# Performance work log

Measured on AMD Instinct MI355X. Metric: run time of the kernel, lower is better.

The kernel has to match this reference:

```python
import jax, jax.numpy as jnp
import numpy as np

B, T, H = 2, 512, 256


def setup_inputs() -> dict:
    key = jax.random.key(0)
    k1, k2, k3, k4, k5 = jax.random.split(key, 5)
    scale = 1.0 / np.sqrt(H)
    Q = jax.random.normal(k1, (B, T, H), dtype=jnp.float32)
    K = jax.random.normal(k2, (B, T, H), dtype=jnp.float32)
    # torch nn.Linear weights: y = x @ W.T, W shape [out, in]
    Wq = jax.random.normal(k3, (H, H), dtype=jnp.float32) * scale
    Wk = jax.random.normal(k4, (H, H), dtype=jnp.float32) * scale
    v = jax.random.normal(k5, (H,), dtype=jnp.float32) * scale  # Linear(H,1) weight
    return {"Q": Q, "K": K, "Wq": Wq, "Wk": Wk, "v": v}


def reference(Q, K, Wq, Wk, v):
    # Project queries and keys: [B,T,H]
    Qp = jnp.einsum("bth,oh->bto", Q, Wq)
    Kp = jnp.einsum("bsh,oh->bso", K, Wk)
    # Additive (Bahdanau) scores: tanh over broadcast sum -> [B,T,T,H], then v-proj -> [B,T,T]
    e = jnp.tanh(Qp[:, :, None, :] + Kp[:, None, :, :])
    scores = jnp.einsum("btsh,h->bts", e, v)
    # Causal mask: query t may only attend to keys s <= t
    mask = jnp.tril(jnp.ones((T, T), dtype=bool))
    scores = jnp.where(mask[None, :, :], scores, jnp.float32(-1e9))
    alpha = jax.nn.softmax(scores, axis=-1)
    # Weighted sum of (raw) K values: [B,T,H]
    ctx = jnp.einsum("bts,bsh->bth", alpha, K)
    return ctx, alpha
```

## Files before the change

### kernel.cpp

```cpp
#include <hip/hip_runtime.h>

#define BB 2
#define TT 512
#define HH 256
#define NBT (BB * TT)

#define C2LOG2E 2.8853900817779268f

__global__ __launch_bounds__(256) void proj_kernel(
    const float* __restrict__ Q, const float* __restrict__ K,
    const float* __restrict__ Wq, const float* __restrict__ Wk,
    float* __restrict__ Eq, float* __restrict__ EkT)
{
    const int ROWS = 8;
    int grp = blockIdx.x;
    const int nQ = NBT / ROWS;
    bool isK = (grp >= nQ);
    int bt0 = (isK ? grp - nQ : grp) * ROWS;
    const float* X = isK ? K : Q;
    const float* W = isK ? Wk : Wq;

    int o = threadIdx.x;
    const float4* w4p = reinterpret_cast<const float4*>(W + o * HH);
    const float4* x4p = reinterpret_cast<const float4*>(X + bt0 * HH);

    float acc[ROWS] = {0.f, 0.f, 0.f, 0.f, 0.f, 0.f, 0.f, 0.f};
#pragma unroll 2
    for (int h4 = 0; h4 < HH / 4; ++h4) {
        float4 w4 = w4p[h4];
#pragma unroll
        for (int r = 0; r < ROWS; ++r) {
            float4 x4 = x4p[r * (HH / 4) + h4];
            acc[r] += x4.x * w4.x + x4.y * w4.y + x4.z * w4.z + x4.w * w4.w;
        }
    }
    if (!isK) {
#pragma unroll
        for (int r = 0; r < ROWS; ++r)
            Eq[(bt0 + r) * HH + o] = __builtin_amdgcn_exp2f(acc[r] * C2LOG2E);
    } else {
        int h4 = o >> 2, c = o & 3;
#pragma unroll
        for (int r = 0; r < ROWS; ++r)
            EkT[(h4 * NBT + bt0 + r) * 4 + c] = __builtin_amdgcn_exp2f(acc[r] * C2LOG2E);
    }
}

__global__ __launch_bounds__(512, 8) void attn_kernel(
    const float* __restrict__ Eq, const float* __restrict__ EkT,
    const float* __restrict__ Kraw, const float* __restrict__ v,
    float* __restrict__ ctx, float* __restrict__ alpha)
{
    int bt = blockIdx.x;
    int b = bt / TT;
    int idx = bt % TT;
    int t = (idx < 256) ? idx : 767 - idx;
    int btr = b * TT + t;
    int tid = threadIdx.x;

    __shared__ float eq_sh[HH];
    __shared__ float v2_sh[HH];
    __shared__ float al_sh[TT];
    __shared__ float red[8];
    __shared__ float4 cred[8][64];

    if (tid < HH) {
        eq_sh[tid] = Eq[btr * HH + tid];
        v2_sh[tid] = -2.0f * v[tid];
    }
    __syncthreads();

    const float4* q4p = reinterpret_cast<const float4*>(eq_sh);
    const float4* v4p = reinterpret_cast<const float4*>(v2_sh);

    float sc = -3.0e38f;
    if (tid <= t) {
        const float4* ek = reinterpret_cast<const float4*>(EkT) + (b * TT + tid);
        float a = 0.f;
#pragma unroll 4
        for (int h4 = 0; h4 < HH / 4; ++h4) {
            float4 e4 = ek[h4 * NBT];
            float4 q4 = q4p[h4];
            float4 vv = v4p[h4];
            float r0 = __builtin_amdgcn_rcpf(__builtin_fmaf(q4.x, e4.x, 1.0f));
            float r1 = __builtin_amdgcn_rcpf(__builtin_fmaf(q4.y, e4.y, 1.0f));
            float r2 = __builtin_amdgcn_rcpf(__builtin_fmaf(q4.z, e4.z, 1.0f));
            float r3 = __builtin_amdgcn_rcpf(__builtin_fmaf(q4.w, e4.w, 1.0f));
            a = __builtin_fmaf(vv.x, r0, a);
            a = __builtin_fmaf(vv.y, r1, a);
            a = __builtin_fmaf(vv.z, r2, a);
            a = __builtin_fmaf(vv.w, r3, a);
        }
        sc = a;
    }

    float m = sc;
#pragma unroll
    for (int off = 32; off > 0; off >>= 1)
        m = fmaxf(m, __shfl_xor(m, off));
    int wid = tid >> 6;
    if ((tid & 63) == 0) red[wid] = m;
    __syncthreads();
    m = fmaxf(fmaxf(fmaxf(red[0], red[1]), fmaxf(red[2], red[3])),
              fmaxf(fmaxf(red[4], red[5]), fmaxf(red[6], red[7])));

    const float LOG2E = 1.4426950408889634f;
    float e = (tid <= t) ? __builtin_amdgcn_exp2f((sc - m) * LOG2E) : 0.f;
    float ssum = e;
#pragma unroll
    for (int off = 32; off > 0; off >>= 1)
        ssum += __shfl_xor(ssum, off);
    __syncthreads();
    if ((tid & 63) == 0) red[wid] = ssum;
    __syncthreads();
    float denom = (red[0] + red[1]) + (red[2] + red[3])
                + (red[4] + red[5]) + (red[6] + red[7]);
    float a0 = e * __builtin_amdgcn_rcpf(denom);

    al_sh[tid] = a0;
    alpha[btr * TT + tid] = a0;
    __syncthreads();

    int hc = tid & 63;
    int sg = tid >> 6;
    const float4* kb4 = reinterpret_cast<const float4*>(Kraw + b * TT * HH) + hc;
    float4 acc4 = {0.f, 0.f, 0.f, 0.f};
#pragma unroll 2
    for (int s = sg; s <= t; s += 8) {
        float4 k4 = kb4[s * 64];
        float  al = al_sh[s];
        acc4.x = __builtin_fmaf(al, k4.x, acc4.x);
        acc4.y = __builtin_fmaf(al, k4.y, acc4.y);
        acc4.z = __builtin_fmaf(al, k4.z, acc4.z);
        acc4.w = __builtin_fmaf(al, k4.w, acc4.w);
    }
    cred[sg][hc] = acc4;
    __syncthreads();
    if (sg == 0) {
        float4 out = {0.f, 0.f, 0.f, 0.f};
#pragma unroll
        for (int g = 0; g < 8; ++g) {
            float4 c = cred[g][hc];
            out.x += c.x; out.y += c.y; out.z += c.z; out.w += c.w;
        }
        reinterpret_cast<float4*>(ctx + btr * HH)[hc] = out;
    }
}

extern "C" void kernel_launch(void* const* d_in, const int* in_sizes, int n_in,
                              void* d_out, int out_size, void* d_ws, size_t ws_size,
                              hipStream_t stream) {
    const float* Q  = (const float*)d_in[0];
    const float* K  = (const float*)d_in[1];
    const float* Wq = (const float*)d_in[2];
    const float* Wk = (const float*)d_in[3];
    const float* v  = (const float*)d_in[4];

    float* ctx   = (float*)d_out;
    float* alpha = (float*)d_out + BB * TT * HH;

    float* Eq  = (float*)d_ws;
    float* EkT = Eq + BB * TT * HH;

    proj_kernel<<<2 * NBT / 8, 256, 0, stream>>>(Q, K, Wq, Wk, Eq, EkT);
    attn_kernel<<<NBT, 512, 0, stream>>>(Eq, EkT, K, v, ctx, alpha);
}
```

Before: 38.85 us.

## Split key transpose into a tiled kernel and drop softmax max reduction

```diff
diff --git a/kernel.cpp b/kernel.cpp
--- a/kernel.cpp
+++ b/kernel.cpp
@@ -6,19 +6,21 @@
 #define NBT (BB * TT)
 
 #define C2LOG2E 2.8853900817779268f
+#define LOG2E   1.4426950408889634f
 
 __global__ __launch_bounds__(256) void proj_kernel(
     const float* __restrict__ Q, const float* __restrict__ K,
     const float* __restrict__ Wq, const float* __restrict__ Wk,
-    float* __restrict__ Eq, float* __restrict__ EkT)
+    float* __restrict__ Eq, float* __restrict__ Ek)
 {
     const int ROWS = 8;
     int grp = blockIdx.x;
-    const int nQ = NBT / ROWS;
+    const int nQ = (BB * TT) / ROWS;
     bool isK = (grp >= nQ);
     int bt0 = (isK ? grp - nQ : grp) * ROWS;
     const float* X = isK ? K : Q;
     const float* W = isK ? Wk : Wq;
+    float* Y = isK ? Ek : Eq;
 
     int o = threadIdx.x;
     const float4* w4p = reinterpret_cast<const float4*>(W + o * HH);
@@ -34,15 +36,37 @@
             acc[r] += x4.x * w4.x + x4.y * w4.y + x4.z * w4.z + x4.w * w4.w;
         }
     }
-    if (!isK) {
 #pragma unroll
-        for (int r = 0; r < ROWS; ++r)
-            Eq[(bt0 + r) * HH + o] = __builtin_amdgcn_exp2f(acc[r] * C2LOG2E);
-    } else {
-        int h4 = o >> 2, c = o & 3;
+    for (int r = 0; r < ROWS; ++r)
+        Y[(bt0 + r) * HH + o] = __builtin_amdgcn_exp2f(acc[r] * C2LOG2E);
+}
+
+__global__ __launch_bounds__(256) void trans_kernel(
+    const float* __restrict__ Ek, float* __restrict__ EkT)
+{
+    __shared__ float t_sh[64][65];
+    int bid = blockIdx.x;
+    int bt0 = (bid & 15) * 64;
+    int h0  = (bid >> 4) * 64;
+    int tid = threadIdx.x;
+    int ty = tid >> 6, tx = tid & 63;
+
 #pragma unroll
-        for (int r = 0; r < ROWS; ++r)
-            EkT[(h4 * NBT + bt0 + r) * 4 + c] = __builtin_amdgcn_exp2f(acc[r] * C2LOG2E);
+    for (int p = 0; p < 16; ++p) {
+        int rr = p * 4 + ty;
+        t_sh[tx][rr] = Ek[(bt0 + rr) * HH + h0 + tx];
+    }
+    __syncthreads();
+#pragma unroll
+    for (int p = 0; p < 4; ++p) {
+        int s = p * 4 + ty;
+        float4 val;
+        val.x = t_sh[s * 4 + 0][tx];
+        val.y = t_sh[s * 4 + 1][tx];
+        val.z = t_sh[s * 4 + 2][tx];
+        val.w = t_sh[s * 4 + 3][tx];
+        *reinterpret_cast<float4*>(
+            EkT + (((h0 >> 2) + s) * NBT + bt0 + tx) * 4) = val;
     }
 }
 
@@ -51,6 +75,12 @@
     const float* __restrict__ Kraw, const float* __restrict__ v,
     float* __restrict__ ctx, float* __restrict__ alpha)
 {
+    __shared__ float eq_sh[HH];
+    __shared__ float v2_sh[HH];
+    __shared__ float al_sh[TT];
+    __shared__ float red[8];
+    __shared__ float4 cred[8][64];
+
     int bt = blockIdx.x;
     int b = bt / TT;
     int idx = bt % TT;
@@ -58,60 +88,39 @@
     int btr = b * TT + t;
     int tid = threadIdx.x;
 
-    __shared__ float eq_sh[HH];
-    __shared__ float v2_sh[HH];
-    __shared__ float al_sh[TT];
-    __shared__ float red[8];
-    __shared__ float4 cred[8][64];
-
     if (tid < HH) {
         eq_sh[tid] = Eq[btr * HH + tid];
         v2_sh[tid] = -2.0f * v[tid];
     }
     __syncthreads();
 
-    const float4* q4p = reinterpret_cast<const float4*>(eq_sh);
-    const float4* v4p = reinterpret_cast<const float4*>(v2_sh);
-
-    float sc = -3.0e38f;
+    float sc = 0.f;
     if (tid <= t) {
         const float4* ek = reinterpret_cast<const float4*>(EkT) + (b * TT + tid);
-        float a = 0.f;
+        const float4* q4p = reinterpret_cast<const float4*>(eq_sh);
+        const float4* v4p = reinterpret_cast<const float4*>(v2_sh);
 #pragma unroll 4
         for (int h4 = 0; h4 < HH / 4; ++h4) {
             float4 e4 = ek[h4 * NBT];
             float4 q4 = q4p[h4];
             float4 vv = v4p[h4];
-            float r0 = __builtin_amdgcn_rcpf(__builtin_fmaf(q4.x, e4.x, 1.0f));
-            float r1 = __builtin_amdgcn_rcpf(__builtin_fmaf(q4.y, e4.y, 1.0f));
-            float r2 = __builtin_amdgcn_rcpf(__builtin_fmaf(q4.z, e4.z, 1.0f));
-            float r3 = __builtin_amdgcn_rcpf(__builtin_fmaf(q4.w, e4.w, 1.0f));
-            a = __builtin_fmaf(vv.x, r0, a);
-            a = __builtin_fmaf(vv.y, r1, a);
-            a = __builtin_fmaf(vv.z, r2, a);
-            a = __builtin_fmaf(vv.w, r3, a);
+            float r0 = __builtin_amdgcn_rcpf(__builtin_fmaf(q4.x, e4.x, 1.f));
+            float r1 = __builtin_amdgcn_rcpf(__builtin_fmaf(q4.y, e4.y, 1.f));
+            float r2 = __builtin_amdgcn_rcpf(__builtin_fmaf(q4.z, e4.z, 1.f));
+            float r3 = __builtin_amdgcn_rcpf(__builtin_fmaf(q4.w, e4.w, 1.f));
+            sc = __builtin_fmaf(vv.x, r0, sc);
+            sc = __builtin_fmaf(vv.y, r1, sc);
+            sc = __builtin_fmaf(vv.z, r2, sc);
+            sc = __builtin_fmaf(vv.w, r3, sc);
         }
-        sc = a;
     }
 
-    float m = sc;
-#pragma unroll
-    for (int off = 32; off > 0; off >>= 1)
-        m = fmaxf(m, __shfl_xor(m, off));
-    int wid = tid >> 6;
-    if ((tid & 63) == 0) red[wid] = m;
-    __syncthreads();
-    m = fmaxf(fmaxf(fmaxf(red[0], red[1]), fmaxf(red[2], red[3])),
-              fmaxf(fmaxf(red[4], red[5]), fmaxf(red[6], red[7])));
-
-    const float LOG2E = 1.4426950408889634f;
-    float e = (tid <= t) ? __builtin_amdgcn_exp2f((sc - m) * LOG2E) : 0.f;
+    float e = (tid <= t) ? __builtin_amdgcn_exp2f(sc * LOG2E) : 0.f;
     float ssum = e;
 #pragma unroll
     for (int off = 32; off > 0; off >>= 1)
         ssum += __shfl_xor(ssum, off);
-    __syncthreads();
-    if ((tid & 63) == 0) red[wid] = ssum;
+    if ((tid & 63) == 0) red[tid >> 6] = ssum;
     __syncthreads();
     float denom = (red[0] + red[1]) + (red[2] + red[3])
                 + (red[4] + red[5]) + (red[6] + red[7]);
@@ -121,11 +130,9 @@
     alpha[btr * TT + tid] = a0;
     __syncthreads();
 
-    int hc = tid & 63;
-    int sg = tid >> 6;
+    int hc = tid & 63, sg = tid >> 6;
     const float4* kb4 = reinterpret_cast<const float4*>(Kraw + b * TT * HH) + hc;
     float4 acc4 = {0.f, 0.f, 0.f, 0.f};
-#pragma unroll 2
     for (int s = sg; s <= t; s += 8) {
         float4 k4 = kb4[s * 64];
         float  al = al_sh[s];
@@ -140,8 +147,8 @@
         float4 out = {0.f, 0.f, 0.f, 0.f};
 #pragma unroll
         for (int g = 0; g < 8; ++g) {
-            float4 c = cred[g][hc];
-            out.x += c.x; out.y += c.y; out.z += c.z; out.w += c.w;
+            float4 cc = cred[g][hc];
+            out.x += cc.x; out.y += cc.y; out.z += cc.z; out.w += cc.w;
         }
         reinterpret_cast<float4*>(ctx + btr * HH)[hc] = out;
     }
@@ -157,11 +164,13 @@
     const float* v  = (const float*)d_in[4];
 
     float* ctx   = (float*)d_out;
-    float* alpha = (float*)d_out + BB * TT * HH;
+    float* alpha = (float*)d_out + NBT * HH;
 
     float* Eq  = (float*)d_ws;
-    float* EkT = Eq + BB * TT * HH;
+    float* Ek  = Eq + NBT * HH;
+    float* EkT = Ek + NBT * HH;
 
-    proj_kernel<<<2 * NBT / 8, 256, 0, stream>>>(Q, K, Wq, Wk, Eq, EkT);
+    proj_kernel<<<256, 256, 0, stream>>>(Q, K, Wq, Wk, Eq, Ek);
+    trans_kernel<<<64, 256, 0, stream>>>(Ek, EkT);
     attn_kernel<<<NBT, 512, 0, stream>>>(Eq, EkT, K, v, ctx, alpha);
 }
```

Measured after the change: 42.98 us. 10.6% more time.
